# Kernel tuning notes

Hardware: AMD Instinct MI355X
Metric: run time of the kernel (lower is better)

## Reference

```python
import jax, jax.numpy as jnp
import numpy as np

OUT_H, OUT_W = 7, 7
SPATIAL_SCALE = 0.25
SAMPLE_NUM = 2
N_ORI = 8
CLOCKWISE = False


def setup_inputs() -> dict:
    key = jax.random.key(0)
    k1, k2, k3, k4, k5 = jax.random.split(key, 5)
    B, Ct, H, W = 2, 256, 256, 256
    n_rois = 512
    features = jax.random.normal(k1, (B, Ct, H, W), dtype=jnp.float32)
    img = H / SPATIAL_SCALE  # image-space extent = 1024
    batch_ind = jax.random.randint(k2, (n_rois,), 0, B).astype(jnp.float32)
    cxy = jax.random.uniform(k3, (n_rois, 2), minval=0.0, maxval=img, dtype=jnp.float32)
    wh = jax.random.uniform(k4, (n_rois, 2), minval=16.0, maxval=img / 4.0, dtype=jnp.float32)
    ang = jax.random.uniform(k5, (n_rois, 1), minval=-np.pi, maxval=np.pi, dtype=jnp.float32)
    rois = jnp.concatenate([batch_ind[:, None], cxy, wh, ang], axis=1)  # (n, 6)
    return {"features": features, "rois": rois}


def _bilinear(feat, y, x):
    # feat: (Ct, H, W); y, x: (P,) -> (Ct, P). Matches mmcv bilinear_interpolate.
    Ct, H, W = feat.shape
    valid = (y >= -1.0) & (y <= H) & (x >= -1.0) & (x <= W)
    y = jnp.maximum(y, 0.0)
    x = jnp.maximum(x, 0.0)
    y0 = jnp.minimum(jnp.floor(y).astype(jnp.int32), H - 1)
    x0 = jnp.minimum(jnp.floor(x).astype(jnp.int32), W - 1)
    y1 = jnp.minimum(y0 + 1, H - 1)
    x1 = jnp.minimum(x0 + 1, W - 1)
    ly = jnp.where(y0 >= H - 1, 0.0, y - y0.astype(y.dtype))
    lx = jnp.where(x0 >= W - 1, 0.0, x - x0.astype(x.dtype))
    hy, hx = 1.0 - ly, 1.0 - lx
    v = ((hy * hx) * feat[:, y0, x0] + (hy * lx) * feat[:, y0, x1]
         + (ly * hx) * feat[:, y1, x0] + (ly * lx) * feat[:, y1, x1])
    return v * valid.astype(feat.dtype)[None, :]


def _per_roi(features, roi):
    B, Ctot, H, W = features.shape
    C = Ctot // N_ORI
    b = roi[0].astype(jnp.int32)
    cx = roi[1] * SPATIAL_SCALE  # roi_center_w
    cy = roi[2] * SPATIAL_SCALE  # roi_center_h
    rw = jnp.maximum(roi[3] * SPATIAL_SCALE, 1.0)
    rh = jnp.maximum(roi[4] * SPATIAL_SCALE, 1.0)
    theta = roi[5]
    bin_h = rh / OUT_H
    bin_w = rw / OUT_W
    # orientation channel alignment (uses un-flipped theta)
    ind_f = theta * N_ORI / (2.0 * jnp.pi)
    ind = jnp.floor(ind_f).astype(jnp.int32)
    l_var = ind_f - ind.astype(theta.dtype)
    r_var = 1.0 - l_var
    ind = jnp.mod(ind, N_ORI)
    th = -theta if CLOCKWISE else theta
    cos_t, sin_t = jnp.cos(th), jnp.sin(th)
    gh = gw = SAMPLE_NUM
    # sample grid in roi-centered coords: yy (OUT_H, gh), xx (OUT_W, gw)
    yy = -rh / 2.0 + (jnp.arange(OUT_H)[:, None] + (jnp.arange(gh) + 0.5) / gh) * bin_h
    xx = -rw / 2.0 + (jnp.arange(OUT_W)[:, None] + (jnp.arange(gw) + 0.5) / gw) * bin_w
    Y = yy[:, None, :, None]  # (OUT_H,1,gh,1)
    X = xx[None, :, None, :]  # (1,OUT_W,1,gw)
    y = (Y * cos_t - X * sin_t + cy).reshape(-1)  # (P,)
    x = (Y * sin_t + X * cos_t + cx).reshape(-1)
    feat = features[b]  # (Ctot, H, W)
    vals = _bilinear(feat, y, x).reshape(C, N_ORI, OUT_H, OUT_W, gh, gw)
    o = jnp.arange(N_ORI)
    idx = jnp.mod(o - ind, N_ORI)
    idx_p = jnp.mod(idx + 1, N_ORI)
    mixed = r_var * vals[:, idx] + l_var * vals[:, idx_p]  # cyclic orientation shift + interp
    out = mixed.mean(axis=(-1, -2))  # average over bin sample grid
    return out.reshape(Ctot, OUT_H, OUT_W)


def reference(features, rois):
    return jax.vmap(lambda r: _per_roi(features, r))(rois)  # (n, Ctot, OUT_H, OUT_W)
```

## Files before the change

kernel.cpp:

```cpp
#include <hip/hip_runtime.h>
#include <hip/hip_fp16.h>
#include <math.h>

#define HH 256
#define WW 256
#define CTOT 256
#define HW (HH * WW)
#define NBIN 49

typedef __attribute__((ext_vector_type(8))) _Float16 half8;
typedef __attribute__((ext_vector_type(4))) float fvec4;

__global__ __launch_bounds__(256) void convert_kernel_v2(
    const float* __restrict__ feats, half8* __restrict__ wsf, int total4 )
{
    const int g = blockIdx.x * 256 + threadIdx.x;
    if (g >= total4) return;
    const int pix = (g & 16383) << 2;
    const int bc  = g >> 14;
    const float* src = feats + ((size_t)bc * 8) * HW + pix;
    fvec4 v[8];
    #pragma unroll
    for (int o = 0; o < 8; ++o)
        v[o] = __builtin_nontemporal_load((const fvec4*)(src + (size_t)o * HW));
    half8* dst = wsf + (size_t)bc * HW + pix;
    #pragma unroll
    for (int j = 0; j < 4; ++j) {
        half8 h;
        h[0] = (_Float16)v[0][j]; h[1] = (_Float16)v[1][j];
        h[2] = (_Float16)v[2][j]; h[3] = (_Float16)v[3][j];
        h[4] = (_Float16)v[4][j]; h[5] = (_Float16)v[5][j];
        h[6] = (_Float16)v[6][j]; h[7] = (_Float16)v[7][j];
        dst[j] = h;
    }
}

__global__ __launch_bounds__(256) void riroi_pool_f16_v3(
    const half8* __restrict__ wsf,
    const float* __restrict__ rois,
    float* __restrict__ out,
    int per_cg4)
{
    const int h = blockIdx.x * 256 + threadIdx.x;
    if (h >= per_cg4) return;
    const int cg  = blockIdx.y;
    const int s   = h & 3;
    const int t   = h >> 2;
    const int n   = t / NBIN;
    const int bin = t - n * NBIN;
    const int ph  = bin / 7;
    const int pw  = bin - ph * 7;

    const float* r = rois + n * 6;
    const int   b     = (int)r[0];
    const float cx    = r[1] * 0.25f;
    const float cy    = r[2] * 0.25f;
    const float rwv   = fmaxf(r[3] * 0.25f, 1.0f);
    const float rhv   = fmaxf(r[4] * 0.25f, 1.0f);
    const float theta = r[5];
    const float bin_h = rhv * (1.0f / 7.0f);
    const float bin_w = rwv * (1.0f / 7.0f);

    const float ind_f = (theta * 8.0f) / 6.28318530717958647692f;
    const int   ind0  = (int)floorf(ind_f);
    const float l_var = ind_f - (float)ind0;
    const float r_var = 1.0f - l_var;
    const int   ind   = ((ind0 % 8) + 8) % 8;
    const float cos_t = cosf(theta);
    const float sin_t = sinf(theta);

    const int gy = s >> 1, gx = s & 1;
    const float yy = -rhv * 0.5f + ((float)ph + ((float)gy + 0.5f) * 0.5f) * bin_h;
    const float xx = -rwv * 0.5f + ((float)pw + ((float)gx + 0.5f) * 0.5f) * bin_w;
    const float y  = yy * cos_t - xx * sin_t + cy;
    const float x  = yy * sin_t + xx * cos_t + cx;
    const float valid =
        (y >= -1.0f && y <= 256.0f && x >= -1.0f && x <= 256.0f) ? 1.0f : 0.0f;
    const float yc = fmaxf(y, 0.0f);
    const float xc = fmaxf(x, 0.0f);
    const int y0 = min((int)floorf(yc), HH - 1);
    const int x0 = min((int)floorf(xc), WW - 1);
    const int y1 = min(y0 + 1, HH - 1);
    const float ly = (y0 >= HH - 1) ? 0.0f : (yc - (float)y0);
    const float lx = (x0 >= WW - 1) ? 0.0f : (xc - (float)x0);
    const float hy = 1.0f - ly, hx = 1.0f - lx;
    const float sc = 0.25f * valid;
    const int   xb = min(x0, WW - 2);
    const float cw0 = (x0 < WW - 1) ? hx : 0.0f;
    const float cw1 = (x0 < WW - 1) ? lx : hx;
    const float w00 = hy * sc * cw0;
    const float w01 = hy * sc * cw1;
    const float w10 = ly * sc * cw0;
    const float w11 = ly * sc * cw1;
    const int off0 = (y0 << 8) + xb;
    const int off1 = (y1 << 8) + xb;

    const half8* base = wsf + (size_t)(b * 32 + cg) * HW;

    const half8 q0 = base[off0];
    const half8 q1 = base[off0 + 1];
    const half8 q2 = base[off1];
    const half8 q3 = base[off1 + 1];

    float acc[8];
    #pragma unroll
    for (int o = 0; o < 8; ++o)
        acc[o] = w00 * (float)q0[o] + w01 * (float)q1[o]
               + w10 * (float)q2[o] + w11 * (float)q3[o];

    #pragma unroll
    for (int o = 0; o < 8; ++o) {
        acc[o] += __shfl_xor(acc[o], 1, 64);
        acc[o] += __shfl_xor(acc[o], 2, 64);
    }

    float* obase = out + ((size_t)n * CTOT + (size_t)(cg * 8)) * NBIN + bin;
    switch (s) {
    case 0:
        __builtin_nontemporal_store(r_var * acc[0] + l_var * acc[1], obase + (((0 + ind) & 7) * NBIN));
        __builtin_nontemporal_store(r_var * acc[1] + l_var * acc[2], obase + (((1 + ind) & 7) * NBIN));
        break;
    case 1:
        __builtin_nontemporal_store(r_var * acc[2] + l_var * acc[3], obase + (((2 + ind) & 7) * NBIN));
        __builtin_nontemporal_store(r_var * acc[3] + l_var * acc[4], obase + (((3 + ind) & 7) * NBIN));
        break;
    case 2:
        __builtin_nontemporal_store(r_var * acc[4] + l_var * acc[5], obase + (((4 + ind) & 7) * NBIN));
        __builtin_nontemporal_store(r_var * acc[5] + l_var * acc[6], obase + (((5 + ind) & 7) * NBIN));
        break;
    default:
        __builtin_nontemporal_store(r_var * acc[6] + l_var * acc[7], obase + (((6 + ind) & 7) * NBIN));
        __builtin_nontemporal_store(r_var * acc[7] + l_var * acc[0], obase + (((7 + ind) & 7) * NBIN));
        break;
    }
}

__global__ __launch_bounds__(256) void riroi_rotated_fallback(
    const float* __restrict__ feats, const float* __restrict__ rois,
    float* __restrict__ out, int total)
{
    const int g = blockIdx.x * 256 + threadIdx.x;
    if (g >= total) return;
    const int wpr = 32 * NBIN;
    const int n   = g / wpr;
    const int rem = g - n * wpr;
    const int cg  = rem / NBIN;
    const int bin = rem - cg * NBIN;
    const int ph  = bin / 7;
    const int pw  = bin - ph * 7;
    const float* r = rois + n * 6;
    const int   b     = (int)r[0];
    const float cx    = r[1] * 0.25f;
    const float cy    = r[2] * 0.25f;
    const float rwv   = fmaxf(r[3] * 0.25f, 1.0f);
    const float rhv   = fmaxf(r[4] * 0.25f, 1.0f);
    const float theta = r[5];
    const float bin_h = rhv * (1.0f / 7.0f);
    const float bin_w = rwv * (1.0f / 7.0f);
    const float ind_f = (theta * 8.0f) / 6.28318530717958647692f;
    const int   ind0  = (int)floorf(ind_f);
    const float l_var = ind_f - (float)ind0;
    const float r_var = 1.0f - l_var;
    const int   ind   = ((ind0 % 8) + 8) % 8;
    const float cos_t = cosf(theta);
    const float sin_t = sinf(theta);
    int   off0[4], off1[4];
    float rw0[4], rw1[4], cw0[4], cw1[4];
    #pragma unroll
    for (int s = 0; s < 4; ++s) {
        const int gy = s >> 1, gx = s & 1;
        const float yy = -rhv * 0.5f + ((float)ph + ((float)gy + 0.5f) * 0.5f) * bin_h;
        const float xx = -rwv * 0.5f + ((float)pw + ((float)gx + 0.5f) * 0.5f) * bin_w;
        const float y  = yy * cos_t - xx * sin_t + cy;
        const float x  = yy * sin_t + xx * cos_t + cx;
        const float valid =
            (y >= -1.0f && y <= 256.0f && x >= -1.0f && x <= 256.0f) ? 1.0f : 0.0f;
        const float yc = fmaxf(y, 0.0f);
        const float xc = fmaxf(x, 0.0f);
        const int y0 = min((int)floorf(yc), HH - 1);
        const int x0 = min((int)floorf(xc), WW - 1);
        const int y1 = min(y0 + 1, HH - 1);
        const float ly = (y0 >= HH - 1) ? 0.0f : (yc - (float)y0);
        const float lx = (x0 >= WW - 1) ? 0.0f : (xc - (float)x0);
        const float hy = 1.0f - ly, hx = 1.0f - lx;
        const float sc = 0.25f * valid;
        const int   xb = min(x0, WW - 2);
        cw0[s]  = (x0 < WW - 1) ? hx : 0.0f;
        cw1[s]  = (x0 < WW - 1) ? lx : hx;
        rw0[s]  = hy * sc;
        rw1[s]  = ly * sc;
        off0[s] = (y0 << 8) + xb;
        off1[s] = (y1 << 8) + xb;
    }
    const float* gbase = feats + (size_t)b * (CTOT * HW) + (size_t)(cg * 8) * HW;
    float acc[8];
    #pragma unroll
    for (int o = 0; o < 8; o += 2) {
        const float* pA = gbase + (size_t)o * HW;
        const float* pB = pA + HW;
        float2 q[16];
        #pragma unroll
        for (int s = 0; s < 4; ++s) {
            q[s * 4 + 0] = *(const float2*)(pA + off0[s]);
            q[s * 4 + 1] = *(const float2*)(pA + off1[s]);
            q[s * 4 + 2] = *(const float2*)(pB + off0[s]);
            q[s * 4 + 3] = *(const float2*)(pB + off1[s]);
        }
        float a0 = 0.0f, a1 = 0.0f;
        #pragma unroll
        for (int s = 0; s < 4; ++s) {
            a0 += rw0[s] * (cw0[s] * q[s * 4 + 0].x + cw1[s] * q[s * 4 + 0].y)
                + rw1[s] * (cw0[s] * q[s * 4 + 1].x + cw1[s] * q[s * 4 + 1].y);
            a1 += rw0[s] * (cw0[s] * q[s * 4 + 2].x + cw1[s] * q[s * 4 + 2].y)
                + rw1[s] * (cw0[s] * q[s * 4 + 3].x + cw1[s] * q[s * 4 + 3].y);
        }
        acc[o] = a0; acc[o + 1] = a1;
    }
    float* obase = out + ((size_t)n * CTOT + (size_t)(cg * 8)) * NBIN + bin;
    #pragma unroll
    for (int s = 0; s < 8; ++s) {
        const int o_out = (s + ind) & 7;
        __builtin_nontemporal_store(r_var * acc[s] + l_var * acc[(s + 1) & 7],
                                    obase + o_out * NBIN);
    }
}

extern "C" void kernel_launch(void* const* d_in, const int* in_sizes, int n_in,
                              void* d_out, int out_size, void* d_ws, size_t ws_size,
                              hipStream_t stream) {
    const float* feats = (const float*)d_in[0];
    const float* rois  = (const float*)d_in[1];
    float* out = (float*)d_out;
    const int n_rois = in_sizes[1] / 6;
    const int B      = in_sizes[0] / (CTOT * HW);
    const size_t ws_need = (size_t)B * 32 * HW * sizeof(half8);

    if (ws_size >= ws_need) {
        half8* wsf = (half8*)d_ws;
        const int tc4 = B * 32 * HW / 4;
        convert_kernel_v2<<<(tc4 + 255) / 256, 256, 0, stream>>>(feats, wsf, tc4);
        const int per_cg4 = n_rois * NBIN * 4;
        dim3 grid((per_cg4 + 255) / 256, 32);
        riroi_pool_f16_v3<<<grid, 256, 0, stream>>>(wsf, rois, out, per_cg4);
    } else {
        const int total = n_rois * 32 * NBIN;
        riroi_rotated_fallback<<<(total + 255) / 256, 256, 0, stream>>>(feats, rois, out, total);
    }
}
```

Baseline: 239.0 us.

## Precompute per-ROI parameter table and process two samples per thread

Adds a small kernel that computes the per-ROI parameters (scaled center/size, cos/sin, orientation index and interpolation weights, batch offset) once into a workspace table, which the pooling kernel reads with vector loads instead of recomputing trig per thread. The pooling kernel now assigns two sample points per thread instead of one, halving the thread count and leaving one shuffle step instead of two. This trades fewer threads and less redundant trig/ALU work for more gathers in flight per thread and an extra kernel launch.

```diff
diff --git a/kernel.cpp b/kernel.cpp
--- a/kernel.cpp
+++ b/kernel.cpp
@@ -10,6 +10,29 @@
 
 typedef __attribute__((ext_vector_type(8))) _Float16 half8;
 typedef __attribute__((ext_vector_type(4))) float fvec4;
+
+__global__ __launch_bounds__(256) void roi_table_kernel(
+    const float* __restrict__ rois, float* __restrict__ tbl, int n_rois)
+{
+    const int n = blockIdx.x * 256 + threadIdx.x;
+    if (n >= n_rois) return;
+    const float* r = rois + n * 6;
+    const float theta = r[5];
+    const float ind_f = (theta * 8.0f) / 6.28318530717958647692f;
+    const int   ind0  = (int)floorf(ind_f);
+    float* o = tbl + n * 12;
+    o[0] = r[1] * 0.25f;
+    o[1] = r[2] * 0.25f;
+    o[2] = fmaxf(r[3] * 0.25f, 1.0f);
+    o[3] = fmaxf(r[4] * 0.25f, 1.0f);
+    o[4] = cosf(theta);
+    o[5] = sinf(theta);
+    o[6] = 1.0f - (ind_f - (float)ind0);
+    o[7] = ind_f - (float)ind0;
+    o[8] = (float)(((ind0 % 8) + 8) % 8);
+    o[9] = (float)(((int)r[0]) * 32);
+    o[10] = 0.0f; o[11] = 0.0f;
+}
 
 __global__ __launch_bounds__(256) void convert_kernel_v2(
     const float* __restrict__ feats, half8* __restrict__ wsf, int total4 )
@@ -35,103 +58,96 @@
     }
 }
 
-__global__ __launch_bounds__(256) void riroi_pool_f16_v3(
+__global__ __launch_bounds__(256) void riroi_pool_f16_v4(
     const half8* __restrict__ wsf,
-    const float* __restrict__ rois,
+    const float* __restrict__ tbl,
     float* __restrict__ out,
-    int per_cg4)
+    int per_cg2)
 {
     const int h = blockIdx.x * 256 + threadIdx.x;
-    if (h >= per_cg4) return;
+    if (h >= per_cg2) return;
     const int cg  = blockIdx.y;
-    const int s   = h & 3;
-    const int t   = h >> 2;
+    const int sh  = h & 1;
+    const int t   = h >> 1;
     const int n   = t / NBIN;
     const int bin = t - n * NBIN;
     const int ph  = bin / 7;
     const int pw  = bin - ph * 7;
 
-    const float* r = rois + n * 6;
-    const int   b     = (int)r[0];
-    const float cx    = r[1] * 0.25f;
-    const float cy    = r[2] * 0.25f;
-    const float rwv   = fmaxf(r[3] * 0.25f, 1.0f);
-    const float rhv   = fmaxf(r[4] * 0.25f, 1.0f);
-    const float theta = r[5];
+    const fvec4 p0 = *(const fvec4*)(tbl + n * 12);
+    const fvec4 p1 = *(const fvec4*)(tbl + n * 12 + 4);
+    const fvec4 p2 = *(const fvec4*)(tbl + n * 12 + 8);
+    const float cx = p0[0], cy = p0[1], rwv = p0[2], rhv = p0[3];
+    const float cos_t = p1[0], sin_t = p1[1], r_var = p1[2], l_var = p1[3];
+    const int   ind = (int)p2[0];
+    const int   b32 = (int)p2[1];
     const float bin_h = rhv * (1.0f / 7.0f);
     const float bin_w = rwv * (1.0f / 7.0f);
 
-    const float ind_f = (theta * 8.0f) / 6.28318530717958647692f;
-    const int   ind0  = (int)floorf(ind_f);
-    const float l_var = ind_f - (float)ind0;
-    const float r_var = 1.0f - l_var;
-    const int   ind   = ((ind0 % 8) + 8) % 8;
-    const float cos_t = cosf(theta);
-    const float sin_t = sinf(theta);
-
-    const int gy = s >> 1, gx = s & 1;
-    const float yy = -rhv * 0.5f + ((float)ph + ((float)gy + 0.5f) * 0.5f) * bin_h;
-    const float xx = -rwv * 0.5f + ((float)pw + ((float)gx + 0.5f) * 0.5f) * bin_w;
-    const float y  = yy * cos_t - xx * sin_t + cy;
-    const float x  = yy * sin_t + xx * cos_t + cx;
-    const float valid =
-        (y >= -1.0f && y <= 256.0f && x >= -1.0f && x <= 256.0f) ? 1.0f : 0.0f;
-    const float yc = fmaxf(y, 0.0f);
-    const float xc = fmaxf(x, 0.0f);
-    const int y0 = min((int)floorf(yc), HH - 1);
-    const int x0 = min((int)floorf(xc), WW - 1);
-    const int y1 = min(y0 + 1, HH - 1);
-    const float ly = (y0 >= HH - 1) ? 0.0f : (yc - (float)y0);
-    const float lx = (x0 >= WW - 1) ? 0.0f : (xc - (float)x0);
-    const float hy = 1.0f - ly, hx = 1.0f - lx;
-    const float sc = 0.25f * valid;
-    const int   xb = min(x0, WW - 2);
-    const float cw0 = (x0 < WW - 1) ? hx : 0.0f;
-    const float cw1 = (x0 < WW - 1) ? lx : hx;
-    const float w00 = hy * sc * cw0;
-    const float w01 = hy * sc * cw1;
-    const float w10 = ly * sc * cw0;
-    const float w11 = ly * sc * cw1;
-    const int off0 = (y0 << 8) + xb;
-    const int off1 = (y1 << 8) + xb;
-
-    const half8* base = wsf + (size_t)(b * 32 + cg) * HW;
-
-    const half8 q0 = base[off0];
-    const half8 q1 = base[off0 + 1];
-    const half8 q2 = base[off1];
-    const half8 q3 = base[off1 + 1];
+    int   off0[2], off1[2];
+    float w00[2], w01[2], w10[2], w11[2];
+    const float yy = -rhv * 0.5f + ((float)ph + ((float)sh + 0.5f) * 0.5f) * bin_h;
+    #pragma unroll
+    for (int j = 0; j < 2; ++j) {
+        const float xx = -rwv * 0.5f + ((float)pw + ((float)j + 0.5f) * 0.5f) * bin_w;
+        const float y  = yy * cos_t - xx * sin_t + cy;
+        const float x  = yy * sin_t + xx * cos_t + cx;
+        const float valid =
+            (y >= -1.0f && y <= 256.0f && x >= -1.0f && x <= 256.0f) ? 1.0f : 0.0f;
+        const float yc = fmaxf(y, 0.0f);
+        const float xc = fmaxf(x, 0.0f);
+        const int y0 = min((int)floorf(yc), HH - 1);
+        const int x0 = min((int)floorf(xc), WW - 1);
+        const int y1 = min(y0 + 1, HH - 1);
+        const float ly = (y0 >= HH - 1) ? 0.0f : (yc - (float)y0);
+        const float lx = (x0 >= WW - 1) ? 0.0f : (xc - (float)x0);
+        const float hy = 1.0f - ly, hx = 1.0f - lx;
+        const float sc = 0.25f * valid;
+        const int   xb = min(x0, WW - 2);
+        const float c0 = (x0 < WW - 1) ? hx : 0.0f;
+        const float c1 = (x0 < WW - 1) ? lx : hx;
+        w00[j] = hy * sc * c0;
+        w01[j] = hy * sc * c1;
+        w10[j] = ly * sc * c0;
+        w11[j] = ly * sc * c1;
+        off0[j] = (y0 << 8) + xb;
+        off1[j] = (y1 << 8) + xb;
+    }
+
+    const half8* base = wsf + (size_t)(b32 + cg) * HW;
+
+    const half8 q0 = base[off0[0]];
+    const half8 q1 = base[off0[0] + 1];
+    const half8 q2 = base[off1[0]];
+    const half8 q3 = base[off1[0] + 1];
+    const half8 q4 = base[off0[1]];
+    const half8 q5 = base[off0[1] + 1];
+    const half8 q6 = base[off1[1]];
+    const half8 q7 = base[off1[1] + 1];
 
     float acc[8];
     #pragma unroll
     for (int o = 0; o < 8; ++o)
-        acc[o] = w00 * (float)q0[o] + w01 * (float)q1[o]
-               + w10 * (float)q2[o] + w11 * (float)q3[o];
-
-    #pragma unroll
-    for (int o = 0; o < 8; ++o) {
+        acc[o] = w00[0] * (float)q0[o] + w01[0] * (float)q1[o]
+               + w10[0] * (float)q2[o] + w11[0] * (float)q3[o]
+               + w00[1] * (float)q4[o] + w01[1] * (float)q5[o]
+               + w10[1] * (float)q6[o] + w11[1] * (float)q7[o];
+
+    #pragma unroll
+    for (int o = 0; o < 8; ++o)
         acc[o] += __shfl_xor(acc[o], 1, 64);
-        acc[o] += __shfl_xor(acc[o], 2, 64);
-    }
 
     float* obase = out + ((size_t)n * CTOT + (size_t)(cg * 8)) * NBIN + bin;
-    switch (s) {
-    case 0:
-        __builtin_nontemporal_store(r_var * acc[0] + l_var * acc[1], obase + (((0 + ind) & 7) * NBIN));
-        __builtin_nontemporal_store(r_var * acc[1] + l_var * acc[2], obase + (((1 + ind) & 7) * NBIN));
-        break;
-    case 1:
-        __builtin_nontemporal_store(r_var * acc[2] + l_var * acc[3], obase + (((2 + ind) & 7) * NBIN));
-        __builtin_nontemporal_store(r_var * acc[3] + l_var * acc[4], obase + (((3 + ind) & 7) * NBIN));
-        break;
-    case 2:
-        __builtin_nontemporal_store(r_var * acc[4] + l_var * acc[5], obase + (((4 + ind) & 7) * NBIN));
-        __builtin_nontemporal_store(r_var * acc[5] + l_var * acc[6], obase + (((5 + ind) & 7) * NBIN));
-        break;
-    default:
-        __builtin_nontemporal_store(r_var * acc[6] + l_var * acc[7], obase + (((6 + ind) & 7) * NBIN));
-        __builtin_nontemporal_store(r_var * acc[7] + l_var * acc[0], obase + (((7 + ind) & 7) * NBIN));
-        break;
+    if (sh == 0) {
+        #pragma unroll
+        for (int k = 0; k < 4; ++k)
+            __builtin_nontemporal_store(r_var * acc[k] + l_var * acc[k + 1],
+                                        obase + (((k + ind) & 7) * NBIN));
+    } else {
+        #pragma unroll
+        for (int k = 4; k < 8; ++k)
+            __builtin_nontemporal_store(r_var * acc[k] + l_var * acc[(k + 1) & 7],
+                                        obase + (((k + ind) & 7) * NBIN));
     }
 }
 
@@ -233,15 +249,18 @@
     float* out = (float*)d_out;
     const int n_rois = in_sizes[1] / 6;
     const int B      = in_sizes[0] / (CTOT * HW);
-    const size_t ws_need = (size_t)B * 32 * HW * sizeof(half8);
-
-    if (ws_size >= ws_need) {
+    const size_t img_bytes = (size_t)B * 32 * HW * sizeof(half8);
+    const size_t tbl_bytes = (size_t)n_rois * 12 * sizeof(float);
+
+    if (ws_size >= img_bytes + tbl_bytes) {
         half8* wsf = (half8*)d_ws;
+        float* tbl = (float*)((char*)d_ws + img_bytes);
+        roi_table_kernel<<<(n_rois + 255) / 256, 256, 0, stream>>>(rois, tbl, n_rois);
         const int tc4 = B * 32 * HW / 4;
         convert_kernel_v2<<<(tc4 + 255) / 256, 256, 0, stream>>>(feats, wsf, tc4);
-        const int per_cg4 = n_rois * NBIN * 4;
-        dim3 grid((per_cg4 + 255) / 256, 32);
-        riroi_pool_f16_v3<<<grid, 256, 0, stream>>>(wsf, rois, out, per_cg4);
+        const int per_cg2 = n_rois * NBIN * 2;
+        dim3 grid((per_cg2 + 255) / 256, 32);
+        riroi_pool_f16_v4<<<grid, 256, 0, stream>>>(wsf, tbl, out, per_cg2);
     } else {
         const int total = n_rois * 32 * NBIN;
         riroi_rotated_fallback<<<(total + 255) / 256, 256, 0, stream>>>(feats, rois, out, total);
```

After: 240.9 us. Within noise of the previous version (+0.8%).
